# Kernel tuning notes

Hardware: AMD Instinct MI355X
Metric: run time of the kernel (lower is better)

The kernel has to match this reference:

```python
import jax, jax.numpy as jnp
import numpy as np

B, N, H, E, D = 8, 2048, 1024, 8, 2048


def setup_inputs() -> dict:
    key = jax.random.key(0)
    k = jax.random.split(key, 5)
    x = jax.random.normal(k[0], (B, N, H), dtype=jnp.float32)
    Wr = jax.random.normal(k[1], (H, E), dtype=jnp.float32) * 0.02
    br = jnp.zeros((E,), dtype=jnp.float32)
    W1 = jax.random.normal(k[2], (E, H, D), dtype=jnp.float32) * 0.02
    b1 = jnp.zeros((E, D), dtype=jnp.float32)
    W2 = jax.random.normal(k[3], (E, D, H), dtype=jnp.float32) * 0.02
    b2 = jnp.zeros((E, H), dtype=jnp.float32)
    return {"x": x, "Wr": Wr, "br": br, "W1": W1, "b1": b1, "W2": W2, "b2": b2}


def reference(x, Wr, br, W1, b1, W2, b2):
    # x: [B,N,H]; router v1, top-1, eval mode (no expert dropout)
    Bx, Nx, Hx = x.shape
    Ex = Wr.shape[1]
    x_flat = x.reshape(Bx * Nx, Hx)                      # [T,H]
    logits = x_flat @ Wr + br                            # [T,E]
    probs = jax.nn.softmax(logits, axis=-1)              # [T,E]
    expert_idx = jnp.argmax(probs, axis=-1)              # [T]

    out_flat = jnp.zeros_like(x_flat)
    for e in range(Ex):  # small fixed loop over experts
        h = jax.nn.gelu(x_flat @ W1[e] + b1[e], approximate=False)  # exact erf GELU (torch default)
        eout = h @ W2[e] + b2[e]                         # [T,H]
        out_flat = jnp.where((expert_idx == e)[:, None], eout, out_flat)

    out = x + out_flat.reshape(Bx, Nx, Hx)               # residual

    p_i = probs.mean(axis=0)                             # [E]
    balance_loss = Ex * jnp.sum(p_i ** 2)
    EPS = 1e-8
    entropy = -jnp.sum(probs * jnp.log(probs + EPS), axis=-1)
    entropy_loss = entropy.mean()
    tokens_per_expert = jnp.bincount(expert_idx, length=Ex)
    return out, balance_loss, entropy_loss, tokens_per_expert
```

## Files before the change

### kernel.cpp

```cpp
#include <hip/hip_runtime.h>
#include <math.h>

#define TT 16384
#define HH 1024
#define DD 2048
#define EE 8
#define MAXTILES 160

typedef float f32x4 __attribute__((ext_vector_type(4)));
typedef __bf16 bf16x8 __attribute__((ext_vector_type(8)));

__device__ __forceinline__ unsigned short f2bf(float f) {
  union { float f; unsigned u; } v; v.f = f;
  unsigned r = v.u + 0x7FFFu + ((v.u >> 16) & 1u);
  return (unsigned short)(r >> 16);
}

__device__ __forceinline__ void gl2lds16(const unsigned short* g, unsigned short* l) {
  __builtin_amdgcn_global_load_lds(
      (const __attribute__((address_space(1))) void*)g,
      (__attribute__((address_space(3))) void*)l, 16, 0, 0);
}

__global__ void k_init(int* counts, float* probs_sum, float* ent_sum) {
  int t = threadIdx.x;
  if (t < EE) { counts[t] = 0; probs_sum[t] = 0.f; }
  if (t == 0) *ent_sum = 0.f;
}

__global__ __launch_bounds__(256) void k_transpose(const float* __restrict__ src,
                                                   unsigned short* __restrict__ dst,
                                                   int R, int C) {
  __shared__ float tile[32][33];
  int tilesC = C / 32, tilesR = R / 32;
  int bid = blockIdx.x;
  int e = bid / (tilesR * tilesC);
  int rem = bid % (tilesR * tilesC);
  int tr = rem / tilesC, tc = rem % tilesC;
  const float* s = src + (size_t)e * R * C;
  unsigned short* d = dst + (size_t)e * R * C;
  int tx = threadIdx.x & 31, ty = threadIdx.x >> 5;
#pragma unroll
  for (int i = 0; i < 4; ++i)
    tile[ty + i * 8][tx] = s[(size_t)(tr * 32 + ty + i * 8) * C + tc * 32 + tx];
  __syncthreads();
#pragma unroll
  for (int i = 0; i < 4; ++i) {
    int rr = ty + i * 8;
    d[(size_t)(tc * 32 + rr) * R + tr * 32 + tx] = f2bf(tile[tx][rr]);
  }
}

__global__ __launch_bounds__(256) void k_router(const float* __restrict__ x,
                                                const float* __restrict__ Wr,
                                                const float* __restrict__ br,
                                                int* __restrict__ eidx,
                                                float* __restrict__ probs_sum,
                                                float* __restrict__ ent_sum,
                                                int* __restrict__ counts,
                                                unsigned short* __restrict__ xb) {
  __shared__ float s_p[EE];
  __shared__ int   s_c[EE];
  __shared__ float s_e;
  int tid = threadIdx.x;
  if (tid < EE) { s_p[tid] = 0.f; s_c[tid] = 0; }
  if (tid == 0) s_e = 0.f;
  __syncthreads();
  int lane = tid & 63, w = tid >> 6;
  for (int tt = 0; tt < 4; ++tt) {
    int token = blockIdx.x * 16 + w * 4 + tt;
    double acc[EE];
#pragma unroll
    for (int e = 0; e < EE; ++e) acc[e] = 0.0;
    const float* xr = x + (size_t)token * HH;
    unsigned short* xo = xb + (size_t)token * HH;
    for (int i = 0; i < 16; ++i) {
      int hh = i * 64 + lane;
      float xf = xr[hh];
      xo[hh] = f2bf(xf);
      double xv = (double)xf;
      const float* wr = Wr + (size_t)hh * EE;
#pragma unroll
      for (int e = 0; e < EE; ++e) acc[e] += xv * (double)wr[e];
    }
#pragma unroll
    for (int off = 32; off > 0; off >>= 1) {
#pragma unroll
      for (int e = 0; e < EE; ++e) acc[e] += __shfl_down(acc[e], off);
    }
    if (lane == 0) {
      double l[EE];
#pragma unroll
      for (int e = 0; e < EE; ++e) l[e] = acc[e] + (double)br[e];
      double m = l[0]; int am = 0;
#pragma unroll
      for (int e = 1; e < EE; ++e) { if (l[e] > m) { m = l[e]; am = e; } }
      double p[EE]; double s = 0.0;
#pragma unroll
      for (int e = 0; e < EE; ++e) { p[e] = exp(l[e] - m); s += p[e]; }
      double inv = 1.0 / s; double ent = 0.0;
#pragma unroll
      for (int e = 0; e < EE; ++e) { p[e] *= inv; ent -= p[e] * log(p[e] + 1e-8); }
      eidx[token] = am;
#pragma unroll
      for (int e = 0; e < EE; ++e) atomicAdd(&s_p[e], (float)p[e]);
      atomicAdd(&s_e, (float)ent);
      atomicAdd(&s_c[am], 1);
    }
  }
  __syncthreads();
  if (tid < EE) { atomicAdd(&probs_sum[tid], s_p[tid]); atomicAdd(&counts[tid], s_c[tid]); }
  if (tid == 0) atomicAdd(ent_sum, s_e);
}

__global__ void k_scan(const int* counts, const float* probs_sum, const float* ent_sum,
                       int* offsets, int* cursor,
                       int* tileE, int* tileR0, int* tileEnd, int* nTiles,
                       float* out_scalars) {
  if (threadIdx.x != 0) return;
  int off = 0, nt = 0;
  for (int e = 0; e < EE; ++e) {
    offsets[e] = off; cursor[e] = off;
    int c = counts[e];
    for (int r = 0; r < c; r += 128) {
      tileE[nt] = e; tileR0[nt] = off + r; tileEnd[nt] = off + c; ++nt;
    }
    off += c;
  }
  offsets[EE] = off;
  *nTiles = nt;
  float bal = 0.f;
  for (int e = 0; e < EE; ++e) { float pi = probs_sum[e] / (float)TT; bal += pi * pi; }
  out_scalars[0] = (float)EE * bal;
  out_scalars[1] = *ent_sum / (float)TT;
  for (int e = 0; e < EE; ++e) out_scalars[2 + e] = (float)counts[e];
}

__global__ __launch_bounds__(256) void k_perm(const int* __restrict__ eidx,
                                              int* cursor, int* __restrict__ perm) {
  int t = blockIdx.x * 256 + threadIdx.x;
  int lane = threadIdx.x & 63;
  int mye = eidx[t];
  int pos = 0;
#pragma unroll
  for (int e = 0; e < EE; ++e) {
    unsigned long long mask = __ballot(mye == e);
    if (mask == 0ull) continue;
    int leader = __ffsll(mask) - 1;
    int base = 0;
    if (lane == leader) base = atomicAdd(&cursor[e], __popcll(mask));
    base = __shfl(base, leader);
    if (mye == e) pos = base + (int)__popcll(mask & ((1ull << lane) - 1ull));
  }
  perm[pos] = t;
}


__global__ __launch_bounds__(256) void k_gemm1(const unsigned short* __restrict__ xb,
                                               const unsigned short* __restrict__ Wt1,
                                               const float* __restrict__ b1,
                                               const int* __restrict__ perm,
                                               const int* __restrict__ tileE,
                                               const int* __restrict__ tileR0,
                                               const int* __restrict__ tileEnd,
                                               const int* __restrict__ nTiles,
                                               unsigned short* __restrict__ hbuf) {
  int tile = blockIdx.y;
  if (tile >= *nTiles) return;
  int e = tileE[tile], r0 = tileR0[tile], rend = tileEnd[tile];
  int c0 = blockIdx.x * 128;
  __shared__ __align__(16) unsigned short As[128 * 32];
  __shared__ __align__(16) unsigned short Bs[128 * 32];
  int tid = threadIdx.x, lane = tid & 63, w = tid >> 6;
  int wr = w >> 1, wc = w & 1;
  int quad = lane >> 4, l16 = lane & 15;
  int srow = lane >> 2, seg = lane & 3;
  int ar0 = w * 32 + srow, ar1 = ar0 + 16;
  int g0 = r0 + ar0; if (g0 >= rend) g0 = rend - 1;
  int g1 = r0 + ar1; if (g1 >= rend) g1 = rend - 1;
  const unsigned short* aG0 = xb + (size_t)perm[g0] * HH + seg * 8;
  const unsigned short* aG1 = xb + (size_t)perm[g1] * HH + seg * 8;
  const unsigned short* bBase = Wt1 + (size_t)e * ((size_t)DD * HH);
  const unsigned short* bG0 = bBase + (size_t)(c0 + ar0) * HH + seg * 8;
  const unsigned short* bG1 = bBase + (size_t)(c0 + ar1) * HH + seg * 8;
  unsigned short* aL0 = &As[(w * 32 + 0) * 32];
  unsigned short* aL1 = &As[(w * 32 + 16) * 32];
  unsigned short* bL0 = &Bs[(w * 32 + 0) * 32];
  unsigned short* bL1 = &Bs[(w * 32 + 16) * 32];
  f32x4 acc[4][4] = {};
  for (int k0 = 0; k0 < HH; k0 += 32) {
    gl2lds16(aG0 + k0, aL0);
    gl2lds16(aG1 + k0, aL1);
    gl2lds16(bG0 + k0, bL0);
    gl2lds16(bG1 + k0, bL1);
    __syncthreads();
    bf16x8 a[4], b[4];
#pragma unroll
    for (int i = 0; i < 4; ++i)
      a[i] = *(const bf16x8*)&As[(wr * 64 + i * 16 + l16) * 32 + quad * 8];
#pragma unroll
    for (int j = 0; j < 4; ++j)
      b[j] = *(const bf16x8*)&Bs[(wc * 64 + j * 16 + l16) * 32 + quad * 8];
#pragma unroll
    for (int i = 0; i < 4; ++i)
#pragma unroll
      for (int j = 0; j < 4; ++j)
        acc[i][j] = __builtin_amdgcn_mfma_f32_16x16x32_bf16(a[i], b[j], acc[i][j], 0, 0, 0);
    __syncthreads();
  }
  float bias[4];
#pragma unroll
  for (int j = 0; j < 4; ++j) bias[j] = b1[e * DD + c0 + wc * 64 + j * 16 + l16];
#pragma unroll
  for (int i = 0; i < 4; ++i) {
#pragma unroll
    for (int r = 0; r < 4; ++r) {
      int gr = r0 + wr * 64 + i * 16 + quad * 4 + r;
      if (gr < rend) {
#pragma unroll
        for (int j = 0; j < 4; ++j) {
          int col = c0 + wc * 64 + j * 16 + l16;
          float v = acc[i][j][r] + bias[j];
          v = 0.5f * v * (1.0f + erff(v * 0.70710678118654752f));
          hbuf[(size_t)gr * DD + col] = f2bf(v);
        }
      }
    }
  }
}

__global__ __launch_bounds__(256) void k_gemm2(const unsigned short* __restrict__ hbuf,
                                               const unsigned short* __restrict__ Wt2,
                                               const float* __restrict__ b2,
                                               const float* __restrict__ x,
                                               const int* __restrict__ perm,
                                               const int* __restrict__ tileE,
                                               const int* __restrict__ tileR0,
                                               const int* __restrict__ tileEnd,
                                               const int* __restrict__ nTiles,
                                               float* __restrict__ outp) {
  int tile = blockIdx.y;
  if (tile >= *nTiles) return;
  int e = tileE[tile], r0 = tileR0[tile], rend = tileEnd[tile];
  int c0 = blockIdx.x * 128;
  __shared__ __align__(16) unsigned short As[128 * 32];
  __shared__ __align__(16) unsigned short Bs[128 * 32];
  int tid = threadIdx.x, lane = tid & 63, w = tid >> 6;
  int wr = w >> 1, wc = w & 1;
  int quad = lane >> 4, l16 = lane & 15;
  int srow = lane >> 2, seg = lane & 3;
  int ar0 = w * 32 + srow, ar1 = ar0 + 16;
  int g0 = r0 + ar0; if (g0 >= rend) g0 = rend - 1;
  int g1 = r0 + ar1; if (g1 >= rend) g1 = rend - 1;
  const unsigned short* aG0 = hbuf + (size_t)g0 * DD + seg * 8;
  const unsigned short* aG1 = hbuf + (size_t)g1 * DD + seg * 8;
  const unsigned short* bBase = Wt2 + (size_t)e * ((size_t)HH * DD);
  const unsigned short* bG0 = bBase + (size_t)(c0 + ar0) * DD + seg * 8;
  const unsigned short* bG1 = bBase + (size_t)(c0 + ar1) * DD + seg * 8;
  unsigned short* aL0 = &As[(w * 32 + 0) * 32];
  unsigned short* aL1 = &As[(w * 32 + 16) * 32];
  unsigned short* bL0 = &Bs[(w * 32 + 0) * 32];
  unsigned short* bL1 = &Bs[(w * 32 + 16) * 32];
  f32x4 acc[4][4] = {};
  for (int k0 = 0; k0 < DD; k0 += 32) {
    gl2lds16(aG0 + k0, aL0);
    gl2lds16(aG1 + k0, aL1);
    gl2lds16(bG0 + k0, bL0);
    gl2lds16(bG1 + k0, bL1);
    __syncthreads();
    bf16x8 a[4], b[4];
#pragma unroll
    for (int i = 0; i < 4; ++i)
      a[i] = *(const bf16x8*)&As[(wr * 64 + i * 16 + l16) * 32 + quad * 8];
#pragma unroll
    for (int j = 0; j < 4; ++j)
      b[j] = *(const bf16x8*)&Bs[(wc * 64 + j * 16 + l16) * 32 + quad * 8];
#pragma unroll
    for (int i = 0; i < 4; ++i)
#pragma unroll
      for (int j = 0; j < 4; ++j)
        acc[i][j] = __builtin_amdgcn_mfma_f32_16x16x32_bf16(a[i], b[j], acc[i][j], 0, 0, 0);
    __syncthreads();
  }
  float bias[4];
#pragma unroll
  for (int j = 0; j < 4; ++j) bias[j] = b2[e * HH + c0 + wc * 64 + j * 16 + l16];
#pragma unroll
  for (int i = 0; i < 4; ++i) {
#pragma unroll
    for (int r = 0; r < 4; ++r) {
      int gr = r0 + wr * 64 + i * 16 + quad * 4 + r;
      if (gr < rend) {
        int tok = perm[gr];
#pragma unroll
        for (int j = 0; j < 4; ++j) {
          int col = c0 + wc * 64 + j * 16 + l16;
          size_t oi = (size_t)tok * HH + col;
          outp[oi] = x[oi] + bias[j] + acc[i][j][r];
        }
      }
    }
  }
}

extern "C" void kernel_launch(void* const* d_in, const int* in_sizes, int n_in,
                              void* d_out, int out_size, void* d_ws, size_t ws_size,
                              hipStream_t stream) {
  const float* x  = (const float*)d_in[0];
  const float* Wr = (const float*)d_in[1];
  const float* br = (const float*)d_in[2];
  const float* W1 = (const float*)d_in[3];
  const float* b1 = (const float*)d_in[4];
  const float* W2 = (const float*)d_in[5];
  const float* b2 = (const float*)d_in[6];
  float* outp = (float*)d_out;

  char* ws = (char*)d_ws;
  int*   counts    = (int*)(ws + 0);
  int*   cursor    = (int*)(ws + 64);
  int*   nTiles    = (int*)(ws + 128);
  float* probs_sum = (float*)(ws + 192);
  float* ent_sum   = (float*)(ws + 256);
  int*   offsets   = (int*)(ws + 320);
  int*   tileE     = (int*)(ws + 512);
  int*   tileR0    = (int*)(ws + 2048);
  int*   tileEnd   = (int*)(ws + 3584);
  int*   eidx      = (int*)(ws + 8192);
  int*   perm      = (int*)(ws + 8192 + 4 * (size_t)TT);
  size_t off = 8192 + 8 * (size_t)TT;
  unsigned short* xb   = (unsigned short*)(ws + off); off += (size_t)TT * HH * 2;
  unsigned short* Wt1  = (unsigned short*)(ws + off); off += (size_t)EE * DD * HH * 2;
  unsigned short* Wt2  = (unsigned short*)(ws + off); off += (size_t)EE * HH * DD * 2;
  unsigned short* hbuf = (unsigned short*)(ws + off); off += (size_t)TT * DD * 2;

  k_init<<<1, 64, 0, stream>>>(counts, probs_sum, ent_sum);
  k_transpose<<<EE * (HH / 32) * (DD / 32), 256, 0, stream>>>(W1, Wt1, HH, DD);
  k_transpose<<<EE * (DD / 32) * (HH / 32), 256, 0, stream>>>(W2, Wt2, DD, HH);
  k_router<<<TT / 16, 256, 0, stream>>>(x, Wr, br, eidx, probs_sum, ent_sum, counts, xb);
  k_scan<<<1, 64, 0, stream>>>(counts, probs_sum, ent_sum, offsets, cursor,
                               tileE, tileR0, tileEnd, nTiles, outp + (size_t)TT * HH);
  k_perm<<<TT / 256, 256, 0, stream>>>(eidx, cursor, perm);
  dim3 g1(DD / 128, MAXTILES);
  k_gemm1<<<g1, 256, 0, stream>>>(xb, Wt1, b1, perm, tileE, tileR0, tileEnd, nTiles, hbuf);
  dim3 g2(HH / 128, MAXTILES);
  k_gemm2<<<g2, 256, 0, stream>>>(hbuf, Wt2, b2, x, perm, tileE, tileR0, tileEnd, nTiles, outp);
}
```

Baseline: 598.1 us.

## Rewrite expert GEMMs with 256x256 tiles, 4-stage LDS pipeline, swizzle, XCD remap

Both expert GEMMs move from 128x128 tiles with 256 threads to 256x256 tiles with 512 threads and 8x4 MFMA accumulators per wave. Global-to-LDS loads now run through a 4-deep buffer ring with explicit vmcnt waits, split A/B prefetch phases, setprio around the MFMA blocks, and an XOR-swizzled LDS layout to avoid bank conflicts. Workgroup IDs are remapped so tiles spread across XCDs, and the scan emits 256-row tiles capped at 96. The goals are more data reuse per byte loaded and global-load latency hidden behind compute. In exchange, register use and LDS use grow (128KB of shared arrays declared per block), and imbalanced experts waste more padded rows per tile.

```diff
diff --git a/kernel.cpp b/kernel.cpp
--- a/kernel.cpp
+++ b/kernel.cpp
@@ -5,7 +5,7 @@
 #define HH 1024
 #define DD 2048
 #define EE 8
-#define MAXTILES 160
+#define MAXT 96
 
 typedef float f32x4 __attribute__((ext_vector_type(4)));
 typedef __bf16 bf16x8 __attribute__((ext_vector_type(8)));
@@ -122,7 +122,7 @@
   for (int e = 0; e < EE; ++e) {
     offsets[e] = off; cursor[e] = off;
     int c = counts[e];
-    for (int r = 0; r < c; r += 128) {
+    for (int r = 0; r < c; r += 256) {
       tileE[nt] = e; tileR0[nt] = off + r; tileEnd[nt] = off + c; ++nt;
     }
     off += c;
@@ -156,66 +156,112 @@
 }
 
 
-__global__ __launch_bounds__(256) void k_gemm1(const unsigned short* __restrict__ xb,
-                                               const unsigned short* __restrict__ Wt1,
-                                               const float* __restrict__ b1,
-                                               const int* __restrict__ perm,
-                                               const int* __restrict__ tileE,
-                                               const int* __restrict__ tileR0,
-                                               const int* __restrict__ tileEnd,
-                                               const int* __restrict__ nTiles,
-                                               unsigned short* __restrict__ hbuf) {
-  int tile = blockIdx.y;
+__global__ __launch_bounds__(512, 2) void k_gemm1(const unsigned short* __restrict__ xb,
+                                                  const unsigned short* __restrict__ Wt1,
+                                                  const float* __restrict__ b1,
+                                                  const int* __restrict__ perm,
+                                                  const int* __restrict__ tileE,
+                                                  const int* __restrict__ tileR0,
+                                                  const int* __restrict__ tileEnd,
+                                                  const int* __restrict__ nTiles,
+                                                  unsigned short* __restrict__ hbuf) {
+  const int gx = DD / 256;
+  const int nwg = gx * MAXT;
+  int wg = blockIdx.y * gx + blockIdx.x;
+  int wgs = (wg & 7) * (nwg >> 3) + (wg >> 3);
+  int tile = wgs / gx, cblk = wgs % gx;
   if (tile >= *nTiles) return;
   int e = tileE[tile], r0 = tileR0[tile], rend = tileEnd[tile];
-  int c0 = blockIdx.x * 128;
-  __shared__ __align__(16) unsigned short As[128 * 32];
-  __shared__ __align__(16) unsigned short Bs[128 * 32];
-  int tid = threadIdx.x, lane = tid & 63, w = tid >> 6;
-  int wr = w >> 1, wc = w & 1;
-  int quad = lane >> 4, l16 = lane & 15;
-  int srow = lane >> 2, seg = lane & 3;
-  int ar0 = w * 32 + srow, ar1 = ar0 + 16;
-  int g0 = r0 + ar0; if (g0 >= rend) g0 = rend - 1;
-  int g1 = r0 + ar1; if (g1 >= rend) g1 = rend - 1;
-  const unsigned short* aG0 = xb + (size_t)perm[g0] * HH + seg * 8;
-  const unsigned short* aG1 = xb + (size_t)perm[g1] * HH + seg * 8;
-  const unsigned short* bBase = Wt1 + (size_t)e * ((size_t)DD * HH);
-  const unsigned short* bG0 = bBase + (size_t)(c0 + ar0) * HH + seg * 8;
-  const unsigned short* bG1 = bBase + (size_t)(c0 + ar1) * HH + seg * 8;
-  unsigned short* aL0 = &As[(w * 32 + 0) * 32];
-  unsigned short* aL1 = &As[(w * 32 + 16) * 32];
-  unsigned short* bL0 = &Bs[(w * 32 + 0) * 32];
-  unsigned short* bL1 = &Bs[(w * 32 + 16) * 32];
-  f32x4 acc[4][4] = {};
-  for (int k0 = 0; k0 < HH; k0 += 32) {
-    gl2lds16(aG0 + k0, aL0);
-    gl2lds16(aG1 + k0, aL1);
-    gl2lds16(bG0 + k0, bL0);
-    gl2lds16(bG1 + k0, bL1);
-    __syncthreads();
-    bf16x8 a[4], b[4];
+  int c0 = cblk * 256;
+
+  __shared__ __align__(16) unsigned short sAB[4][2][8192];
+
+  int tid = threadIdx.x, lane = tid & 63, wid = tid >> 6;
+  int wr = wid >> 2, wc = wid & 3;
+  int l16 = lane & 15, quad = lane >> 4;
+  const int fsw  = (quad ^ ((l16 >> 1) & 3)) << 3;
+  const int aoff = (wr * 128 + l16) * 32 + fsw;
+  const int boff = (wc * 64 + l16) * 32 + fsw;
+
+  int srow = lane >> 2;
+  const int ssw = (((lane & 3) ^ ((lane >> 3) & 3)) << 3);
+  int ra0 = r0 + wid * 16 + srow;        if (ra0 > rend - 1) ra0 = rend - 1;
+  int ra1 = r0 + wid * 16 + 128 + srow;  if (ra1 > rend - 1) ra1 = rend - 1;
+  const unsigned short* aS0 = xb + (size_t)perm[ra0] * HH + ssw;
+  const unsigned short* aS1 = xb + (size_t)perm[ra1] * HH + ssw;
+  const unsigned short* bB  = Wt1 + (size_t)e * DD * HH;
+  const unsigned short* bS0 = bB + (size_t)(c0 + wid * 16 + srow) * HH + ssw;
+  const unsigned short* bS1 = bB + (size_t)(c0 + wid * 16 + 128 + srow) * HH + ssw;
+  const int dA0 = wid * 512, dA1 = wid * 512 + 4096;
+
+  f32x4 acc[8][4] = {};
+  const int NT = HH / 32;
+
+#pragma unroll
+  for (int t = 0; t < 3; ++t) {
+    gl2lds16(aS0 + t * 32, &sAB[t][0][dA0]);
+    gl2lds16(aS1 + t * 32, &sAB[t][0][dA1]);
+    gl2lds16(bS0 + t * 32, &sAB[t][1][dA0]);
+    gl2lds16(bS1 + t * 32, &sAB[t][1][dA1]);
+  }
+  asm volatile("s_waitcnt vmcnt(8)" ::: "memory");
+  __builtin_amdgcn_s_barrier();
+
+#pragma unroll 4
+  for (int kt = 0; kt < NT; ++kt) {
+    const unsigned short* A = &sAB[kt & 3][0][0];
+    const unsigned short* B = &sAB[kt & 3][1][0];
+    int ts = kt + 3;
+    bf16x8 av[4], bv[4];
+    if (ts < NT) {
+      gl2lds16(aS0 + ts * 32, &sAB[ts & 3][0][dA0]);
+      gl2lds16(aS1 + ts * 32, &sAB[ts & 3][0][dA1]);
+    }
+#pragma unroll
+    for (int i = 0; i < 4; ++i) av[i] = *(const bf16x8*)(A + aoff + i * 512);
+#pragma unroll
+    for (int j = 0; j < 4; ++j) bv[j] = *(const bf16x8*)(B + boff + j * 512);
+    __builtin_amdgcn_s_barrier();
+    asm volatile("s_waitcnt lgkmcnt(0)");
+    __builtin_amdgcn_sched_barrier(0);
+    __builtin_amdgcn_s_setprio(1);
 #pragma unroll
     for (int i = 0; i < 4; ++i)
-      a[i] = *(const bf16x8*)&As[(wr * 64 + i * 16 + l16) * 32 + quad * 8];
-#pragma unroll
-    for (int j = 0; j < 4; ++j)
-      b[j] = *(const bf16x8*)&Bs[(wc * 64 + j * 16 + l16) * 32 + quad * 8];
+#pragma unroll
+      for (int j = 0; j < 4; ++j)
+        acc[i][j] = __builtin_amdgcn_mfma_f32_16x16x32_bf16(av[i], bv[j], acc[i][j], 0, 0, 0);
+    __builtin_amdgcn_s_setprio(0);
+    __builtin_amdgcn_s_barrier();
+    if (ts < NT) {
+      gl2lds16(bS0 + ts * 32, &sAB[ts & 3][1][dA0]);
+      gl2lds16(bS1 + ts * 32, &sAB[ts & 3][1][dA1]);
+    }
+#pragma unroll
+    for (int i = 0; i < 4; ++i) av[i] = *(const bf16x8*)(A + aoff + (i + 4) * 512);
+    __builtin_amdgcn_s_barrier();
+    asm volatile("s_waitcnt lgkmcnt(0)");
+    __builtin_amdgcn_sched_barrier(0);
+    __builtin_amdgcn_s_setprio(1);
 #pragma unroll
     for (int i = 0; i < 4; ++i)
 #pragma unroll
       for (int j = 0; j < 4; ++j)
-        acc[i][j] = __builtin_amdgcn_mfma_f32_16x16x32_bf16(a[i], b[j], acc[i][j], 0, 0, 0);
-    __syncthreads();
-  }
+        acc[i + 4][j] = __builtin_amdgcn_mfma_f32_16x16x32_bf16(av[i], bv[j], acc[i + 4][j], 0, 0, 0);
+    __builtin_amdgcn_s_setprio(0);
+    if (kt < NT - 3)       asm volatile("s_waitcnt vmcnt(8)" ::: "memory");
+    else if (kt == NT - 3) asm volatile("s_waitcnt vmcnt(4)" ::: "memory");
+    else if (kt == NT - 2) asm volatile("s_waitcnt vmcnt(0)" ::: "memory");
+    __builtin_amdgcn_s_barrier();
+  }
+
   float bias[4];
 #pragma unroll
   for (int j = 0; j < 4; ++j) bias[j] = b1[e * DD + c0 + wc * 64 + j * 16 + l16];
 #pragma unroll
-  for (int i = 0; i < 4; ++i) {
+  for (int i = 0; i < 8; ++i) {
 #pragma unroll
     for (int r = 0; r < 4; ++r) {
-      int gr = r0 + wr * 64 + i * 16 + quad * 4 + r;
+      int gr = r0 + wr * 128 + i * 16 + quad * 4 + r;
       if (gr < rend) {
 #pragma unroll
         for (int j = 0; j < 4; ++j) {
@@ -229,67 +275,113 @@
   }
 }
 
-__global__ __launch_bounds__(256) void k_gemm2(const unsigned short* __restrict__ hbuf,
-                                               const unsigned short* __restrict__ Wt2,
-                                               const float* __restrict__ b2,
-                                               const float* __restrict__ x,
-                                               const int* __restrict__ perm,
-                                               const int* __restrict__ tileE,
-                                               const int* __restrict__ tileR0,
-                                               const int* __restrict__ tileEnd,
-                                               const int* __restrict__ nTiles,
-                                               float* __restrict__ outp) {
-  int tile = blockIdx.y;
+__global__ __launch_bounds__(512, 2) void k_gemm2(const unsigned short* __restrict__ hbuf,
+                                                  const unsigned short* __restrict__ Wt2,
+                                                  const float* __restrict__ b2,
+                                                  const float* __restrict__ x,
+                                                  const int* __restrict__ perm,
+                                                  const int* __restrict__ tileE,
+                                                  const int* __restrict__ tileR0,
+                                                  const int* __restrict__ tileEnd,
+                                                  const int* __restrict__ nTiles,
+                                                  float* __restrict__ outp) {
+  const int gx = HH / 256;
+  const int nwg = gx * MAXT;
+  int wg = blockIdx.y * gx + blockIdx.x;
+  int wgs = (wg & 7) * (nwg >> 3) + (wg >> 3);
+  int tile = wgs / gx, cblk = wgs % gx;
   if (tile >= *nTiles) return;
   int e = tileE[tile], r0 = tileR0[tile], rend = tileEnd[tile];
-  int c0 = blockIdx.x * 128;
-  __shared__ __align__(16) unsigned short As[128 * 32];
-  __shared__ __align__(16) unsigned short Bs[128 * 32];
-  int tid = threadIdx.x, lane = tid & 63, w = tid >> 6;
-  int wr = w >> 1, wc = w & 1;
-  int quad = lane >> 4, l16 = lane & 15;
-  int srow = lane >> 2, seg = lane & 3;
-  int ar0 = w * 32 + srow, ar1 = ar0 + 16;
-  int g0 = r0 + ar0; if (g0 >= rend) g0 = rend - 1;
-  int g1 = r0 + ar1; if (g1 >= rend) g1 = rend - 1;
-  const unsigned short* aG0 = hbuf + (size_t)g0 * DD + seg * 8;
-  const unsigned short* aG1 = hbuf + (size_t)g1 * DD + seg * 8;
-  const unsigned short* bBase = Wt2 + (size_t)e * ((size_t)HH * DD);
-  const unsigned short* bG0 = bBase + (size_t)(c0 + ar0) * DD + seg * 8;
-  const unsigned short* bG1 = bBase + (size_t)(c0 + ar1) * DD + seg * 8;
-  unsigned short* aL0 = &As[(w * 32 + 0) * 32];
-  unsigned short* aL1 = &As[(w * 32 + 16) * 32];
-  unsigned short* bL0 = &Bs[(w * 32 + 0) * 32];
-  unsigned short* bL1 = &Bs[(w * 32 + 16) * 32];
-  f32x4 acc[4][4] = {};
-  for (int k0 = 0; k0 < DD; k0 += 32) {
-    gl2lds16(aG0 + k0, aL0);
-    gl2lds16(aG1 + k0, aL1);
-    gl2lds16(bG0 + k0, bL0);
-    gl2lds16(bG1 + k0, bL1);
-    __syncthreads();
-    bf16x8 a[4], b[4];
+  int c0 = cblk * 256;
+
+  __shared__ __align__(16) unsigned short sAB[4][2][8192];
+
+  int tid = threadIdx.x, lane = tid & 63, wid = tid >> 6;
+  int wr = wid >> 2, wc = wid & 3;
+  int l16 = lane & 15, quad = lane >> 4;
+  const int fsw  = (quad ^ ((l16 >> 1) & 3)) << 3;
+  const int aoff = (wr * 128 + l16) * 32 + fsw;
+  const int boff = (wc * 64 + l16) * 32 + fsw;
+
+  int srow = lane >> 2;
+  const int ssw = (((lane & 3) ^ ((lane >> 3) & 3)) << 3);
+  int ra0 = r0 + wid * 16 + srow;        if (ra0 > rend - 1) ra0 = rend - 1;
+  int ra1 = r0 + wid * 16 + 128 + srow;  if (ra1 > rend - 1) ra1 = rend - 1;
+  const unsigned short* aS0 = hbuf + (size_t)ra0 * DD + ssw;
+  const unsigned short* aS1 = hbuf + (size_t)ra1 * DD + ssw;
+  const unsigned short* bB  = Wt2 + (size_t)e * HH * DD;
+  const unsigned short* bS0 = bB + (size_t)(c0 + wid * 16 + srow) * DD + ssw;
+  const unsigned short* bS1 = bB + (size_t)(c0 + wid * 16 + 128 + srow) * DD + ssw;
+  const int dA0 = wid * 512, dA1 = wid * 512 + 4096;
+
+  f32x4 acc[8][4] = {};
+  const int NT = DD / 32;
+
+#pragma unroll
+  for (int t = 0; t < 3; ++t) {
+    gl2lds16(aS0 + t * 32, &sAB[t][0][dA0]);
+    gl2lds16(aS1 + t * 32, &sAB[t][0][dA1]);
+    gl2lds16(bS0 + t * 32, &sAB[t][1][dA0]);
+    gl2lds16(bS1 + t * 32, &sAB[t][1][dA1]);
+  }
+  asm volatile("s_waitcnt vmcnt(8)" ::: "memory");
+  __builtin_amdgcn_s_barrier();
+
+#pragma unroll 4
+  for (int kt = 0; kt < NT; ++kt) {
+    const unsigned short* A = &sAB[kt & 3][0][0];
+    const unsigned short* B = &sAB[kt & 3][1][0];
+    int ts = kt + 3;
+    bf16x8 av[4], bv[4];
+    if (ts < NT) {
+      gl2lds16(aS0 + ts * 32, &sAB[ts & 3][0][dA0]);
+      gl2lds16(aS1 + ts * 32, &sAB[ts & 3][0][dA1]);
+    }
+#pragma unroll
+    for (int i = 0; i < 4; ++i) av[i] = *(const bf16x8*)(A + aoff + i * 512);
+#pragma unroll
+    for (int j = 0; j < 4; ++j) bv[j] = *(const bf16x8*)(B + boff + j * 512);
+    __builtin_amdgcn_s_barrier();
+    asm volatile("s_waitcnt lgkmcnt(0)");
+    __builtin_amdgcn_sched_barrier(0);
+    __builtin_amdgcn_s_setprio(1);
 #pragma unroll
     for (int i = 0; i < 4; ++i)
-      a[i] = *(const bf16x8*)&As[(wr * 64 + i * 16 + l16) * 32 + quad * 8];
-#pragma unroll
-    for (int j = 0; j < 4; ++j)
-      b[j] = *(const bf16x8*)&Bs[(wc * 64 + j * 16 + l16) * 32 + quad * 8];
+#pragma unroll
+      for (int j = 0; j < 4; ++j)
+        acc[i][j] = __builtin_amdgcn_mfma_f32_16x16x32_bf16(av[i], bv[j], acc[i][j], 0, 0, 0);
+    __builtin_amdgcn_s_setprio(0);
+    __builtin_amdgcn_s_barrier();
+    if (ts < NT) {
+      gl2lds16(bS0 + ts * 32, &sAB[ts & 3][1][dA0]);
+      gl2lds16(bS1 + ts * 32, &sAB[ts & 3][1][dA1]);
+    }
+#pragma unroll
+    for (int i = 0; i < 4; ++i) av[i] = *(const bf16x8*)(A + aoff + (i + 4) * 512);
+    __builtin_amdgcn_s_barrier();
+    asm volatile("s_waitcnt lgkmcnt(0)");
+    __builtin_amdgcn_sched_barrier(0);
+    __builtin_amdgcn_s_setprio(1);
 #pragma unroll
     for (int i = 0; i < 4; ++i)
 #pragma unroll
       for (int j = 0; j < 4; ++j)
-        acc[i][j] = __builtin_amdgcn_mfma_f32_16x16x32_bf16(a[i], b[j], acc[i][j], 0, 0, 0);
-    __syncthreads();
-  }
+        acc[i + 4][j] = __builtin_amdgcn_mfma_f32_16x16x32_bf16(av[i], bv[j], acc[i + 4][j], 0, 0, 0);
+    __builtin_amdgcn_s_setprio(0);
+    if (kt < NT - 3)       asm volatile("s_waitcnt vmcnt(8)" ::: "memory");
+    else if (kt == NT - 3) asm volatile("s_waitcnt vmcnt(4)" ::: "memory");
+    else if (kt == NT - 2) asm volatile("s_waitcnt vmcnt(0)" ::: "memory");
+    __builtin_amdgcn_s_barrier();
+  }
+
   float bias[4];
 #pragma unroll
   for (int j = 0; j < 4; ++j) bias[j] = b2[e * HH + c0 + wc * 64 + j * 16 + l16];
 #pragma unroll
-  for (int i = 0; i < 4; ++i) {
+  for (int i = 0; i < 8; ++i) {
 #pragma unroll
     for (int r = 0; r < 4; ++r) {
-      int gr = r0 + wr * 64 + i * 16 + quad * 4 + r;
+      int gr = r0 + wr * 128 + i * 16 + quad * 4 + r;
       if (gr < rend) {
         int tok = perm[gr];
 #pragma unroll
@@ -340,8 +432,8 @@
   k_scan<<<1, 64, 0, stream>>>(counts, probs_sum, ent_sum, offsets, cursor,
                                tileE, tileR0, tileEnd, nTiles, outp + (size_t)TT * HH);
   k_perm<<<TT / 256, 256, 0, stream>>>(eidx, cursor, perm);
-  dim3 g1(DD / 128, MAXTILES);
-  k_gemm1<<<g1, 256, 0, stream>>>(xb, Wt1, b1, perm, tileE, tileR0, tileEnd, nTiles, hbuf);
-  dim3 g2(HH / 128, MAXTILES);
-  k_gemm2<<<g2, 256, 0, stream>>>(hbuf, Wt2, b2, x, perm, tileE, tileR0, tileEnd, nTiles, outp);
-}
+  dim3 g1(DD / 256, MAXT);
+  k_gemm1<<<g1, 512, 0, stream>>>(xb, Wt1, b1, perm, tileE, tileR0, tileEnd, nTiles, hbuf);
+  dim3 g2(HH / 256, MAXT);
+  k_gemm2<<<g2, 512, 0, stream>>>(hbuf, Wt2, b2, x, perm, tileE, tileR0, tileEnd, nTiles, outp);
+}
```

Result: slower. 631.8 us (+5.6%).

## Double-buffer LDS in expert GEMMs with 256-row tiles, 512 threads and swizzle

Applied to the files above, without the earlier changes.

Both grouped expert GEMMs move to 256x128 tiles run by 512 threads (8 waves, each still owning a 64x64 sub-tile). LDS buffers are doubled so the next k-slice's global-to-LDS loads are issued before the current slice's MFMAs, with one barrier per iteration instead of two. An XOR swizzle on LDS row segments reduces bank conflicts, and setprio favours the MFMA waves. Larger row tiles mean more padding waste on each expert's partial last tile, and the tile count cap drops to 96.

```diff
diff --git a/kernel.cpp b/kernel.cpp
--- a/kernel.cpp
+++ b/kernel.cpp
@@ -5,7 +5,7 @@
 #define HH 1024
 #define DD 2048
 #define EE 8
-#define MAXTILES 160
+#define MAXT 96
 
 typedef float f32x4 __attribute__((ext_vector_type(4)));
 typedef __bf16 bf16x8 __attribute__((ext_vector_type(8)));
@@ -122,7 +122,7 @@
   for (int e = 0; e < EE; ++e) {
     offsets[e] = off; cursor[e] = off;
     int c = counts[e];
-    for (int r = 0; r < c; r += 128) {
+    for (int r = 0; r < c; r += 256) {
       tileE[nt] = e; tileR0[nt] = off + r; tileEnd[nt] = off + c; ++nt;
     }
     off += c;
@@ -156,58 +156,75 @@
 }
 
 
-__global__ __launch_bounds__(256) void k_gemm1(const unsigned short* __restrict__ xb,
-                                               const unsigned short* __restrict__ Wt1,
-                                               const float* __restrict__ b1,
-                                               const int* __restrict__ perm,
-                                               const int* __restrict__ tileE,
-                                               const int* __restrict__ tileR0,
-                                               const int* __restrict__ tileEnd,
-                                               const int* __restrict__ nTiles,
-                                               unsigned short* __restrict__ hbuf) {
-  int tile = blockIdx.y;
+__global__ __launch_bounds__(512, 4) void k_gemm1(const unsigned short* __restrict__ xb,
+                                                  const unsigned short* __restrict__ Wt1,
+                                                  const float* __restrict__ b1,
+                                                  const int* __restrict__ perm,
+                                                  const int* __restrict__ tileE,
+                                                  const int* __restrict__ tileR0,
+                                                  const int* __restrict__ tileEnd,
+                                                  const int* __restrict__ nTiles,
+                                                  unsigned short* __restrict__ hbuf) {
+  int tile = blockIdx.y, cblk = blockIdx.x;
   if (tile >= *nTiles) return;
   int e = tileE[tile], r0 = tileR0[tile], rend = tileEnd[tile];
-  int c0 = blockIdx.x * 128;
-  __shared__ __align__(16) unsigned short As[128 * 32];
-  __shared__ __align__(16) unsigned short Bs[128 * 32];
-  int tid = threadIdx.x, lane = tid & 63, w = tid >> 6;
-  int wr = w >> 1, wc = w & 1;
-  int quad = lane >> 4, l16 = lane & 15;
-  int srow = lane >> 2, seg = lane & 3;
-  int ar0 = w * 32 + srow, ar1 = ar0 + 16;
-  int g0 = r0 + ar0; if (g0 >= rend) g0 = rend - 1;
-  int g1 = r0 + ar1; if (g1 >= rend) g1 = rend - 1;
-  const unsigned short* aG0 = xb + (size_t)perm[g0] * HH + seg * 8;
-  const unsigned short* aG1 = xb + (size_t)perm[g1] * HH + seg * 8;
-  const unsigned short* bBase = Wt1 + (size_t)e * ((size_t)DD * HH);
-  const unsigned short* bG0 = bBase + (size_t)(c0 + ar0) * HH + seg * 8;
-  const unsigned short* bG1 = bBase + (size_t)(c0 + ar1) * HH + seg * 8;
-  unsigned short* aL0 = &As[(w * 32 + 0) * 32];
-  unsigned short* aL1 = &As[(w * 32 + 16) * 32];
-  unsigned short* bL0 = &Bs[(w * 32 + 0) * 32];
-  unsigned short* bL1 = &Bs[(w * 32 + 16) * 32];
+  int c0 = cblk * 128;
+
+  __shared__ __align__(16) unsigned short sA[2][256 * 32];
+  __shared__ __align__(16) unsigned short sB[2][128 * 32];
+
+  int tid = threadIdx.x, lane = tid & 63, wid = tid >> 6;
+  int wr = wid >> 1, wc = wid & 1;
+  int l16 = lane & 15, quad = lane >> 4;
+  const int fsw  = (quad ^ ((l16 >> 1) & 3)) << 3;
+  const int aoff = (wr * 64 + l16) * 32 + fsw;
+  const int boff = (wc * 64 + l16) * 32 + fsw;
+
+  const int ssw = (((tid & 3) ^ ((tid >> 3) & 3)) << 3);
+  int row0 = r0 + (tid >> 2);        if (row0 > rend - 1) row0 = rend - 1;
+  int row1 = r0 + 128 + (tid >> 2);  if (row1 > rend - 1) row1 = rend - 1;
+  const unsigned short* aG0 = xb + (size_t)perm[row0] * HH + ssw;
+  const unsigned short* aG1 = xb + (size_t)perm[row1] * HH + ssw;
+  const unsigned short* bG  = Wt1 + (size_t)e * DD * HH + (size_t)(c0 + (tid >> 2)) * HH + ssw;
+  const int dstA0 = wid * 512, dstA1 = 4096 + wid * 512, dstB = wid * 512;
+
   f32x4 acc[4][4] = {};
-  for (int k0 = 0; k0 < HH; k0 += 32) {
-    gl2lds16(aG0 + k0, aL0);
-    gl2lds16(aG1 + k0, aL1);
-    gl2lds16(bG0 + k0, bL0);
-    gl2lds16(bG1 + k0, bL1);
-    __syncthreads();
-    bf16x8 a[4], b[4];
+  const int NT = HH / 32;
+
+  gl2lds16(aG0, &sA[0][dstA0]);
+  gl2lds16(aG1, &sA[0][dstA1]);
+  gl2lds16(bG,  &sB[0][dstB]);
+  asm volatile("s_waitcnt vmcnt(0)" ::: "memory");
+  __builtin_amdgcn_s_barrier();
+
+#pragma unroll 2
+  for (int kt = 0; kt < NT; ++kt) {
+    const unsigned short* A = &sA[kt & 1][0];
+    const unsigned short* B = &sB[kt & 1][0];
+    bf16x8 av[4], bv[4];
+#pragma unroll
+    for (int i = 0; i < 4; ++i) av[i] = *(const bf16x8*)(A + aoff + i * 512);
+#pragma unroll
+    for (int j = 0; j < 4; ++j) bv[j] = *(const bf16x8*)(B + boff + j * 512);
+    if (kt + 1 < NT) {
+      int nb = (kt + 1) & 1, ko = (kt + 1) * 32;
+      gl2lds16(aG0 + ko, &sA[nb][dstA0]);
+      gl2lds16(aG1 + ko, &sA[nb][dstA1]);
+      gl2lds16(bG  + ko, &sB[nb][dstB]);
+    }
+    asm volatile("s_waitcnt lgkmcnt(0)");
+    __builtin_amdgcn_sched_barrier(0);
+    __builtin_amdgcn_s_setprio(1);
 #pragma unroll
     for (int i = 0; i < 4; ++i)
-      a[i] = *(const bf16x8*)&As[(wr * 64 + i * 16 + l16) * 32 + quad * 8];
-#pragma unroll
-    for (int j = 0; j < 4; ++j)
-      b[j] = *(const bf16x8*)&Bs[(wc * 64 + j * 16 + l16) * 32 + quad * 8];
-#pragma unroll
-    for (int i = 0; i < 4; ++i)
 #pragma unroll
       for (int j = 0; j < 4; ++j)
-        acc[i][j] = __builtin_amdgcn_mfma_f32_16x16x32_bf16(a[i], b[j], acc[i][j], 0, 0, 0);
-    __syncthreads();
-  }
+        acc[i][j] = __builtin_amdgcn_mfma_f32_16x16x32_bf16(av[i], bv[j], acc[i][j], 0, 0, 0);
+    __builtin_amdgcn_s_setprio(0);
+    asm volatile("s_waitcnt vmcnt(0)" ::: "memory");
+    __builtin_amdgcn_s_barrier();
+  }
+
   float bias[4];
 #pragma unroll
   for (int j = 0; j < 4; ++j) bias[j] = b1[e * DD + c0 + wc * 64 + j * 16 + l16];
@@ -229,59 +246,76 @@
   }
 }
 
-__global__ __launch_bounds__(256) void k_gemm2(const unsigned short* __restrict__ hbuf,
-                                               const unsigned short* __restrict__ Wt2,
-                                               const float* __restrict__ b2,
-                                               const float* __restrict__ x,
-                                               const int* __restrict__ perm,
-                                               const int* __restrict__ tileE,
-                                               const int* __restrict__ tileR0,
-                                               const int* __restrict__ tileEnd,
-                                               const int* __restrict__ nTiles,
-                                               float* __restrict__ outp) {
-  int tile = blockIdx.y;
+__global__ __launch_bounds__(512, 4) void k_gemm2(const unsigned short* __restrict__ hbuf,
+                                                  const unsigned short* __restrict__ Wt2,
+                                                  const float* __restrict__ b2,
+                                                  const float* __restrict__ x,
+                                                  const int* __restrict__ perm,
+                                                  const int* __restrict__ tileE,
+                                                  const int* __restrict__ tileR0,
+                                                  const int* __restrict__ tileEnd,
+                                                  const int* __restrict__ nTiles,
+                                                  float* __restrict__ outp) {
+  int tile = blockIdx.y, cblk = blockIdx.x;
   if (tile >= *nTiles) return;
   int e = tileE[tile], r0 = tileR0[tile], rend = tileEnd[tile];
-  int c0 = blockIdx.x * 128;
-  __shared__ __align__(16) unsigned short As[128 * 32];
-  __shared__ __align__(16) unsigned short Bs[128 * 32];
-  int tid = threadIdx.x, lane = tid & 63, w = tid >> 6;
-  int wr = w >> 1, wc = w & 1;
-  int quad = lane >> 4, l16 = lane & 15;
-  int srow = lane >> 2, seg = lane & 3;
-  int ar0 = w * 32 + srow, ar1 = ar0 + 16;
-  int g0 = r0 + ar0; if (g0 >= rend) g0 = rend - 1;
-  int g1 = r0 + ar1; if (g1 >= rend) g1 = rend - 1;
-  const unsigned short* aG0 = hbuf + (size_t)g0 * DD + seg * 8;
-  const unsigned short* aG1 = hbuf + (size_t)g1 * DD + seg * 8;
-  const unsigned short* bBase = Wt2 + (size_t)e * ((size_t)HH * DD);
-  const unsigned short* bG0 = bBase + (size_t)(c0 + ar0) * DD + seg * 8;
-  const unsigned short* bG1 = bBase + (size_t)(c0 + ar1) * DD + seg * 8;
-  unsigned short* aL0 = &As[(w * 32 + 0) * 32];
-  unsigned short* aL1 = &As[(w * 32 + 16) * 32];
-  unsigned short* bL0 = &Bs[(w * 32 + 0) * 32];
-  unsigned short* bL1 = &Bs[(w * 32 + 16) * 32];
+  int c0 = cblk * 128;
+
+  __shared__ __align__(16) unsigned short sA[2][256 * 32];
+  __shared__ __align__(16) unsigned short sB[2][128 * 32];
+
+  int tid = threadIdx.x, lane = tid & 63, wid = tid >> 6;
+  int wr = wid >> 1, wc = wid & 1;
+  int l16 = lane & 15, quad = lane >> 4;
+  const int fsw  = (quad ^ ((l16 >> 1) & 3)) << 3;
+  const int aoff = (wr * 64 + l16) * 32 + fsw;
+  const int boff = (wc * 64 + l16) * 32 + fsw;
+
+  const int ssw = (((tid & 3) ^ ((tid >> 3) & 3)) << 3);
+  int row0 = r0 + (tid >> 2);        if (row0 > rend - 1) row0 = rend - 1;
+  int row1 = r0 + 128 + (tid >> 2);  if (row1 > rend - 1) row1 = rend - 1;
+  const unsigned short* aG0 = hbuf + (size_t)row0 * DD + ssw;
+  const unsigned short* aG1 = hbuf + (size_t)row1 * DD + ssw;
+  const unsigned short* bG  = Wt2 + (size_t)e * HH * DD + (size_t)(c0 + (tid >> 2)) * DD + ssw;
+  const int dstA0 = wid * 512, dstA1 = 4096 + wid * 512, dstB = wid * 512;
+
   f32x4 acc[4][4] = {};
-  for (int k0 = 0; k0 < DD; k0 += 32) {
-    gl2lds16(aG0 + k0, aL0);
-    gl2lds16(aG1 + k0, aL1);
-    gl2lds16(bG0 + k0, bL0);
-    gl2lds16(bG1 + k0, bL1);
-    __syncthreads();
-    bf16x8 a[4], b[4];
+  const int NT = DD / 32;
+
+  gl2lds16(aG0, &sA[0][dstA0]);
+  gl2lds16(aG1, &sA[0][dstA1]);
+  gl2lds16(bG,  &sB[0][dstB]);
+  asm volatile("s_waitcnt vmcnt(0)" ::: "memory");
+  __builtin_amdgcn_s_barrier();
+
+#pragma unroll 2
+  for (int kt = 0; kt < NT; ++kt) {
+    const unsigned short* A = &sA[kt & 1][0];
+    const unsigned short* B = &sB[kt & 1][0];
+    bf16x8 av[4], bv[4];
+#pragma unroll
+    for (int i = 0; i < 4; ++i) av[i] = *(const bf16x8*)(A + aoff + i * 512);
+#pragma unroll
+    for (int j = 0; j < 4; ++j) bv[j] = *(const bf16x8*)(B + boff + j * 512);
+    if (kt + 1 < NT) {
+      int nb = (kt + 1) & 1, ko = (kt + 1) * 32;
+      gl2lds16(aG0 + ko, &sA[nb][dstA0]);
+      gl2lds16(aG1 + ko, &sA[nb][dstA1]);
+      gl2lds16(bG  + ko, &sB[nb][dstB]);
+    }
+    asm volatile("s_waitcnt lgkmcnt(0)");
+    __builtin_amdgcn_sched_barrier(0);
+    __builtin_amdgcn_s_setprio(1);
 #pragma unroll
     for (int i = 0; i < 4; ++i)
-      a[i] = *(const bf16x8*)&As[(wr * 64 + i * 16 + l16) * 32 + quad * 8];
-#pragma unroll
-    for (int j = 0; j < 4; ++j)
-      b[j] = *(const bf16x8*)&Bs[(wc * 64 + j * 16 + l16) * 32 + quad * 8];
-#pragma unroll
-    for (int i = 0; i < 4; ++i)
 #pragma unroll
       for (int j = 0; j < 4; ++j)
-        acc[i][j] = __builtin_amdgcn_mfma_f32_16x16x32_bf16(a[i], b[j], acc[i][j], 0, 0, 0);
-    __syncthreads();
-  }
+        acc[i][j] = __builtin_amdgcn_mfma_f32_16x16x32_bf16(av[i], bv[j], acc[i][j], 0, 0, 0);
+    __builtin_amdgcn_s_setprio(0);
+    asm volatile("s_waitcnt vmcnt(0)" ::: "memory");
+    __builtin_amdgcn_s_barrier();
+  }
+
   float bias[4];
 #pragma unroll
   for (int j = 0; j < 4; ++j) bias[j] = b2[e * HH + c0 + wc * 64 + j * 16 + l16];
@@ -340,8 +374,8 @@
   k_scan<<<1, 64, 0, stream>>>(counts, probs_sum, ent_sum, offsets, cursor,
                                tileE, tileR0, tileEnd, nTiles, outp + (size_t)TT * HH);
   k_perm<<<TT / 256, 256, 0, stream>>>(eidx, cursor, perm);
-  dim3 g1(DD / 128, MAXTILES);
-  k_gemm1<<<g1, 256, 0, stream>>>(xb, Wt1, b1, perm, tileE, tileR0, tileEnd, nTiles, hbuf);
-  dim3 g2(HH / 128, MAXTILES);
-  k_gemm2<<<g2, 256, 0, stream>>>(hbuf, Wt2, b2, x, perm, tileE, tileR0, tileEnd, nTiles, outp);
-}
+  dim3 g1(DD / 128, MAXT);
+  k_gemm1<<<g1, 512, 0, stream>>>(xb, Wt1, b1, perm, tileE, tileR0, tileEnd, nTiles, hbuf);
+  dim3 g2(HH / 128, MAXT);
+  k_gemm2<<<g2, 512, 0, stream>>>(hbuf, Wt2, b2, x, perm, tileE, tileR0, tileEnd, nTiles, outp);
+}
```

After: 599.2 us. Within noise of the previous version (+0.2%).
